# Kernel tuning notes

Hardware: AMD Instinct MI355X
Metric: run time of the kernel (lower is better)

## Reference

```python
import jax, jax.numpy as jnp
import numpy as np

N, D, TRIALS = 8192, 256, 150  # batch size, embed dim, max mining trials (count < 150)


def setup_inputs() -> dict:
    key = jax.random.key(0)
    k1, k2, k3, k4 = jax.random.split(key, 4)
    return {
        "batch_hd": jax.random.normal(k1, (N, D), jnp.float32),
        "batch_tgt": jax.random.randint(k2, (N,), 0, 2, jnp.int32),  # 0 = genuine, 1 = spoof
        "margin": jnp.ones((1,), jnp.float32),
        "u_pos": jax.random.uniform(k3, (N,), jnp.float32),          # uniform for positive pick
        "u_neg": jax.random.uniform(k4, (N, TRIALS), jnp.float32),   # uniforms for 150 negative trials
    }


def reference(batch_hd, batch_tgt, margin, u_pos, u_neg):
    n = batch_hd.shape[0]
    # squared-L2 pairwise distance matrix: ||a||^2 - 2 a.b + ||b||^2  -> [N, N]
    sq = jnp.sum(batch_hd * batch_hd, axis=-1)
    dst = sq[:, None] - 2.0 * (batch_hd @ batch_hd.T) + sq[None, :]

    is_genu = batch_tgt == 0
    n_genu = jnp.sum(is_genu.astype(jnp.int32))
    n_spoof = jnp.int32(n) - n_genu
    # per-anchor pool sizes (original indexes dst_mat with the RAW randint, so only sizes matter)
    len_pos = jnp.where(is_genu, n_genu, n_spoof)
    len_neg = jnp.where(is_genu, n_spoof, n_genu)

    idx = jnp.arange(n, dtype=jnp.int32)
    # positive: uniform over [0, len_pos) excluding the anchor index (only possible when idx < len_pos)
    excl = idx < len_pos
    eff = len_pos - excl.astype(jnp.int32)  # effective pool size after exclusion, >= 1 by assert
    u = jnp.minimum((u_pos * eff).astype(jnp.int32), eff - 1)
    pos_idx = u + (excl & (u >= idx)).astype(jnp.int32)

    # negatives: 150 pre-drawn uniform trials per anchor -> raw indices in [0, len_neg)
    neg_cand = jnp.minimum((u_neg * len_neg[:, None]).astype(jnp.int32), len_neg[:, None] - 1)

    dst_pos = dst[idx, pos_idx]                             # [N]
    dst_neg = jnp.take_along_axis(dst, neg_cand, axis=1)    # [N, TRIALS] (row i = anchor i)

    # break condition: dst_pos < dst_neg and dst_pos - dst_neg + margin > 0 (semi-hard)
    cond = (dst_pos[:, None] < dst_neg) & ((dst_pos[:, None] - dst_neg + margin[0]) > 0)
    first_hit = jnp.argmax(cond, axis=1)          # first trial satisfying the break
    # fallback: strict '<' update == first occurrence of the min (argmin semantics)
    first_min = jnp.argmin(dst_neg, axis=1)
    t = jnp.where(cond.any(axis=1), first_hit, first_min)
    neg_idx = jnp.take_along_axis(neg_cand, t[:, None], axis=1)[:, 0]

    # stack([hd[anch], hd[pos], hd[neg]]).transpose(0,1) -> [N, 3, D]
    return jnp.stack([batch_hd, batch_hd[pos_idx], batch_hd[neg_idx]], axis=1)
```

## Files before the change

kernel.cpp:

```cpp
#include <hip/hip_runtime.h>

#define BN 8192
#define BD 256
#define NTRIALS 150

__device__ __forceinline__ float wave_reduce_sum(float v) {
    #pragma unroll
    for (int m = 32; m > 0; m >>= 1) v += __shfl_xor(v, m, 64);
    return v;
}

__global__ __launch_bounds__(1024) void count_genuine_kernel(
    const int* __restrict__ tgt, int* __restrict__ cnt)
{
    __shared__ int lds[16];
    const int t = threadIdx.x;
    int c = 0;
    for (int i = t; i < BN; i += 1024) c += (tgt[i] == 0) ? 1 : 0;
    #pragma unroll
    for (int m = 32; m > 0; m >>= 1) c += __shfl_xor(c, m, 64);
    if ((t & 63) == 0) lds[t >> 6] = c;
    __syncthreads();
    if (t == 0) {
        int s = 0;
        #pragma unroll
        for (int w = 0; w < 16; ++w) s += lds[w];
        *cnt = s;
    }
}

__global__ __launch_bounds__(256) void sqnorm_kernel(
    const float* __restrict__ hd, float* __restrict__ sq)
{
    const int lane = threadIdx.x & 63;
    const int row  = blockIdx.x * 4 + (threadIdx.x >> 6);
    const float4 a = *reinterpret_cast<const float4*>(hd + row * BD + lane * 4);
    float s = a.x * a.x + a.y * a.y + a.z * a.z + a.w * a.w;
    s = wave_reduce_sum(s);
    if (lane == 0) sq[row] = s;
}

#define TRIAL_COMPUTE_PF(CSLOT, BJSLOT, SQSLOT, PFT, CSAVE, DNSAVE)             \
    {                                                                           \
        const int    c_  = CSLOT;                                               \
        const float4 bj  = BJSLOT;                                              \
        const float  sqc = SQSLOT;                                              \
        {                                                                       \
            int c2 = (int)(unrow[PFT] * lnf);                                   \
            c2 = min(c2, lnm1);                                                 \
            CSLOT  = c2;                                                        \
            BJSLOT = *reinterpret_cast<const float4*>(hd + c2 * BD + lane * 4); \
            SQSLOT = sq[c2];                                                    \
        }                                                                       \
        float p = a.x * bj.x + a.y * bj.y + a.z * bj.z + a.w * bj.w;            \
        const float dn = (sqi - 2.0f * wave_reduce_sum(p)) + sqc;               \
        CSAVE  = c_;                                                            \
        DNSAVE = dn;                                                            \
    }

#define TRIAL_COMPUTE_NP(CSLOT, BJSLOT, SQSLOT, CSAVE, DNSAVE)                  \
    {                                                                           \
        const int    c_  = CSLOT;                                               \
        const float4 bj  = BJSLOT;                                              \
        const float  sqc = SQSLOT;                                              \
        float p = a.x * bj.x + a.y * bj.y + a.z * bj.z + a.w * bj.w;            \
        const float dn = (sqi - 2.0f * wave_reduce_sum(p)) + sqc;               \
        CSAVE  = c_;                                                            \
        DNSAVE = dn;                                                            \
    }

#define TRIAL_CHECK(CSAVE, DNSAVE)                                              \
    {                                                                           \
        const float z = dst_pos - (DNSAVE);                                     \
        if ((z < 0.0f) && (z + margin > 0.0f)) { chosen = (CSAVE); goto done; } \
        if ((DNSAVE) < best) { best = (DNSAVE); best_c = (CSAVE); }             \
    }

__global__ __launch_bounds__(256) void triplet_kernel(
    const float* __restrict__ hd, const int* __restrict__ tgt,
    const float* __restrict__ margin_p, const float* __restrict__ u_pos,
    const float* __restrict__ u_neg, const float* __restrict__ sq,
    const int* __restrict__ cnt, float* __restrict__ out)
{
    const int lane = threadIdx.x & 63;
    const int i    = blockIdx.x * 4 + (threadIdx.x >> 6);

    const float4 a = *reinterpret_cast<const float4*>(hd + i * BD + lane * 4);
    const float sqi = sq[i];

    const int ng = *cnt;
    const int ti = tgt[i];
    const int len_pos = (ti == 0) ? ng : (BN - ng);
    const int len_neg = (ti == 0) ? (BN - ng) : ng;

    const bool excl = (i < len_pos);
    const int  eff  = len_pos - (excl ? 1 : 0);
    const float up  = u_pos[i];
    int u = (int)(up * (float)eff);
    u = min(u, eff - 1);
    const int pos_idx = u + ((excl && (u >= i)) ? 1 : 0);

    const float4 bp = *reinterpret_cast<const float4*>(hd + pos_idx * BD + lane * 4);
    float pp = a.x * bp.x + a.y * bp.y + a.z * bp.z + a.w * bp.w;
    const float dot_pos = wave_reduce_sum(pp);
    const float dst_pos = (sqi - 2.0f * dot_pos) + sq[pos_idx];

    float* orow = out + i * (3 * BD);
    *reinterpret_cast<float4*>(orow + lane * 4) = a;
    *reinterpret_cast<float4*>(orow + BD + lane * 4) = bp;

    const float margin = margin_p[0];
    const float lnf    = (float)len_neg;
    const int   lnm1   = len_neg - 1;

    int   chosen = -1;
    float best   = __builtin_inff();
    int   best_c = 0;
    const float* unrow = u_neg + i * NTRIALS;

    int cA, cB, cC; float4 bjA, bjB, bjC; float sqA, sqB, sqC;
    {
        int c = (int)(unrow[0] * lnf);
        c = min(c, lnm1);
        cA = c;
        bjA = *reinterpret_cast<const float4*>(hd + c * BD + lane * 4);
        sqA = sq[c];
    }
    {
        int c = (int)(unrow[1] * lnf);
        c = min(c, lnm1);
        cB = c;
        bjB = *reinterpret_cast<const float4*>(hd + c * BD + lane * 4);
        sqB = sq[c];
    }
    {
        int c = (int)(unrow[2] * lnf);
        c = min(c, lnm1);
        cC = c;
        bjC = *reinterpret_cast<const float4*>(hd + c * BD + lane * 4);
        sqC = sq[c];
    }

    for (int t = 0; t < NTRIALS - 3; t += 3) {
        int cs0, cs1, cs2;
        float dn0, dn1, dn2;
        TRIAL_COMPUTE_PF(cA, bjA, sqA, t + 3, cs0, dn0)
        TRIAL_COMPUTE_PF(cB, bjB, sqB, t + 4, cs1, dn1)
        TRIAL_COMPUTE_PF(cC, bjC, sqC, t + 5, cs2, dn2)
        TRIAL_CHECK(cs0, dn0)
        TRIAL_CHECK(cs1, dn1)
        TRIAL_CHECK(cs2, dn2)
    }
    {
        int cs0, cs1, cs2;
        float dn0, dn1, dn2;
        TRIAL_COMPUTE_NP(cA, bjA, sqA, cs0, dn0)
        TRIAL_COMPUTE_NP(cB, bjB, sqB, cs1, dn1)
        TRIAL_COMPUTE_NP(cC, bjC, sqC, cs2, dn2)
        TRIAL_CHECK(cs0, dn0)
        TRIAL_CHECK(cs1, dn1)
        TRIAL_CHECK(cs2, dn2)
    }
done:
    ;
    const int neg = (chosen >= 0) ? chosen : best_c;

    const float4 bn = *reinterpret_cast<const float4*>(hd + neg * BD + lane * 4);
    *reinterpret_cast<float4*>(orow + 2 * BD + lane * 4) = bn;
}

extern "C" void kernel_launch(void* const* d_in, const int* in_sizes, int n_in,
                              void* d_out, int out_size, void* d_ws, size_t ws_size,
                              hipStream_t stream) {
    const float* hd     = (const float*)d_in[0];
    const int*   tgt    = (const int*)d_in[1];
    const float* margin = (const float*)d_in[2];
    const float* u_pos  = (const float*)d_in[3];
    const float* u_neg  = (const float*)d_in[4];
    float* out = (float*)d_out;

    float* sq  = (float*)d_ws;
    int*   cnt = (int*)((char*)d_ws + BN * sizeof(float));

    count_genuine_kernel<<<1, 1024, 0, stream>>>(tgt, cnt);
    sqnorm_kernel<<<BN / 4, 256, 0, stream>>>(hd, sq);
    triplet_kernel<<<BN / 4, 256, 0, stream>>>(hd, tgt, margin, u_pos, u_neg, sq, cnt, out);
}
```

Before: 90.96 us.

## Split each anchor's negative-mining trials across two waves with early-exit flag

Each anchor is now handled by two waves, each scanning half of the 150 negative trials, with results merged through shared memory. The second half polls an LDS flag set when the first half finds a semi-hard hit, so it can stop early. This shortens the serial per-wave trial chain, at the cost of doubling the block count, redundant positive/anchor work per wave, and speculative trials in the second half that may be wasted.

```diff
diff --git a/kernel.cpp b/kernel.cpp
--- a/kernel.cpp
+++ b/kernel.cpp
@@ -3,6 +3,7 @@
 #define BN 8192
 #define BD 256
 #define NTRIALS 150
+#define HALF 75
 
 __device__ __forceinline__ float wave_reduce_sum(float v) {
     #pragma unroll
@@ -76,14 +77,34 @@
         if ((DNSAVE) < best) { best = (DNSAVE); best_c = (CSAVE); }             \
     }
 
+#define PROLOGUE_SLOT(CS, BJS, SQS, T)                                          \
+    {                                                                           \
+        int c = (int)(unrow[T] * lnf);                                          \
+        c = min(c, lnm1);                                                       \
+        CS  = c;                                                                \
+        BJS = *reinterpret_cast<const float4*>(hd + c * BD + lane * 4);         \
+        SQS = sq[c];                                                            \
+    }
+
 __global__ __launch_bounds__(256) void triplet_kernel(
     const float* __restrict__ hd, const int* __restrict__ tgt,
     const float* __restrict__ margin_p, const float* __restrict__ u_pos,
     const float* __restrict__ u_neg, const float* __restrict__ sq,
     const int* __restrict__ cnt, float* __restrict__ out)
 {
+    __shared__ int   s_chosen[2][2];
+    __shared__ float s_best[2][2];
+    __shared__ int   s_bestc[2][2];
+    __shared__ int   s_aflag[2];
+
     const int lane = threadIdx.x & 63;
-    const int i    = blockIdx.x * 4 + (threadIdx.x >> 6);
+    const int w    = threadIdx.x >> 6;
+    const int ancl = w >> 1;
+    const int half = w & 1;
+    const int i    = blockIdx.x * 2 + ancl;
+
+    if (threadIdx.x < 2) s_aflag[threadIdx.x] = 0;
+    __syncthreads();
 
     const float4 a = *reinterpret_cast<const float4*>(hd + i * BD + lane * 4);
     const float sqi = sq[i];
@@ -106,8 +127,10 @@
     const float dst_pos = (sqi - 2.0f * dot_pos) + sq[pos_idx];
 
     float* orow = out + i * (3 * BD);
-    *reinterpret_cast<float4*>(orow + lane * 4) = a;
-    *reinterpret_cast<float4*>(orow + BD + lane * 4) = bp;
+    if (half == 0) {
+        *reinterpret_cast<float4*>(orow + lane * 4) = a;
+        *reinterpret_cast<float4*>(orow + BD + lane * 4) = bp;
+    }
 
     const float margin = margin_p[0];
     const float lnf    = (float)len_neg;
@@ -116,57 +139,63 @@
     int   chosen = -1;
     float best   = __builtin_inff();
     int   best_c = 0;
-    const float* unrow = u_neg + i * NTRIALS;
-
-    int cA, cB, cC; float4 bjA, bjB, bjC; float sqA, sqB, sqC;
+    const float* unrow = u_neg + i * NTRIALS + half * HALF;
+
     {
-        int c = (int)(unrow[0] * lnf);
-        c = min(c, lnm1);
-        cA = c;
-        bjA = *reinterpret_cast<const float4*>(hd + c * BD + lane * 4);
-        sqA = sq[c];
-    }
-    {
-        int c = (int)(unrow[1] * lnf);
-        c = min(c, lnm1);
-        cB = c;
-        bjB = *reinterpret_cast<const float4*>(hd + c * BD + lane * 4);
-        sqB = sq[c];
-    }
-    {
-        int c = (int)(unrow[2] * lnf);
-        c = min(c, lnm1);
-        cC = c;
-        bjC = *reinterpret_cast<const float4*>(hd + c * BD + lane * 4);
-        sqC = sq[c];
-    }
-
-    for (int t = 0; t < NTRIALS - 3; t += 3) {
-        int cs0, cs1, cs2;
-        float dn0, dn1, dn2;
-        TRIAL_COMPUTE_PF(cA, bjA, sqA, t + 3, cs0, dn0)
-        TRIAL_COMPUTE_PF(cB, bjB, sqB, t + 4, cs1, dn1)
-        TRIAL_COMPUTE_PF(cC, bjC, sqC, t + 5, cs2, dn2)
-        TRIAL_CHECK(cs0, dn0)
-        TRIAL_CHECK(cs1, dn1)
-        TRIAL_CHECK(cs2, dn2)
-    }
-    {
-        int cs0, cs1, cs2;
-        float dn0, dn1, dn2;
-        TRIAL_COMPUTE_NP(cA, bjA, sqA, cs0, dn0)
-        TRIAL_COMPUTE_NP(cB, bjB, sqB, cs1, dn1)
-        TRIAL_COMPUTE_NP(cC, bjC, sqC, cs2, dn2)
-        TRIAL_CHECK(cs0, dn0)
-        TRIAL_CHECK(cs1, dn1)
-        TRIAL_CHECK(cs2, dn2)
+        int cA, cB, cC; float4 bjA, bjB, bjC; float sqA, sqB, sqC;
+        PROLOGUE_SLOT(cA, bjA, sqA, 0)
+        PROLOGUE_SLOT(cB, bjB, sqB, 1)
+        PROLOGUE_SLOT(cC, bjC, sqC, 2)
+
+        for (int t = 0; t < HALF - 3; t += 3) {
+            int cs0, cs1, cs2;
+            float dn0, dn1, dn2;
+            TRIAL_COMPUTE_PF(cA, bjA, sqA, t + 3, cs0, dn0)
+            TRIAL_COMPUTE_PF(cB, bjB, sqB, t + 4, cs1, dn1)
+            TRIAL_COMPUTE_PF(cC, bjC, sqC, t + 5, cs2, dn2)
+            TRIAL_CHECK(cs0, dn0)
+            TRIAL_CHECK(cs1, dn1)
+            TRIAL_CHECK(cs2, dn2)
+            if (half && *(volatile int*)&s_aflag[ancl]) goto bail;
+        }
+        {
+            int cs0, cs1, cs2;
+            float dn0, dn1, dn2;
+            TRIAL_COMPUTE_NP(cA, bjA, sqA, cs0, dn0)
+            TRIAL_COMPUTE_NP(cB, bjB, sqB, cs1, dn1)
+            TRIAL_COMPUTE_NP(cC, bjC, sqC, cs2, dn2)
+            TRIAL_CHECK(cs0, dn0)
+            TRIAL_CHECK(cs1, dn1)
+            TRIAL_CHECK(cs2, dn2)
+        }
     }
 done:
-    ;
-    const int neg = (chosen >= 0) ? chosen : best_c;
-
-    const float4 bn = *reinterpret_cast<const float4*>(hd + neg * BD + lane * 4);
-    *reinterpret_cast<float4*>(orow + 2 * BD + lane * 4) = bn;
+    if (half == 0 && chosen >= 0 && lane == 0) *(volatile int*)&s_aflag[ancl] = 1;
+bail:
+    if (lane == 0) {
+        s_chosen[ancl][half] = chosen;
+        s_best[ancl][half]   = best;
+        s_bestc[ancl][half]  = best_c;
+    }
+    __syncthreads();
+
+    if (half == 0) {
+        const int chA = s_chosen[ancl][0];
+        const int chB = s_chosen[ancl][1];
+        int neg;
+        if (chA >= 0) {
+            neg = chA;
+        } else if (chB >= 0) {
+            neg = chB;
+        } else {
+            const float bA = s_best[ancl][0];
+            const float bB = s_best[ancl][1];
+            neg = (bB < bA) ? s_bestc[ancl][1]
+                            : s_bestc[ancl][0];
+        }
+        const float4 bn = *reinterpret_cast<const float4*>(hd + neg * BD + lane * 4);
+        *reinterpret_cast<float4*>(orow + 2 * BD + lane * 4) = bn;
+    }
 }
 
 extern "C" void kernel_launch(void* const* d_in, const int* in_sizes, int n_in,
@@ -184,5 +213,5 @@
 
     count_genuine_kernel<<<1, 1024, 0, stream>>>(tgt, cnt);
     sqnorm_kernel<<<BN / 4, 256, 0, stream>>>(hd, sq);
-    triplet_kernel<<<BN / 4, 256, 0, stream>>>(hd, tgt, margin, u_pos, u_neg, sq, cnt, out);
-}
+    triplet_kernel<<<BN / 2, 256, 0, stream>>>(hd, tgt, margin, u_pos, u_neg, sq, cnt, out);
+}
```

Measured after the change: 88.57 us. 1.03x faster.
